# Optimization experiments

Measured on AMD Instinct MI355X. Metric: run time of the kernel, lower is better.

Reference implementation:

```python
import jax, jax.numpy as jnp
import numpy as np

DIM = 2048            # model dim
HID = 4096            # ssm inner dim (multiple_of*round(2/3*6144))
H = 64                # n_heads
P = HID // H          # head_dim = 64
N = 128               # state_dim
G = 1                 # n_groups
K = 4                 # conv_size
Q = 128               # chunk_size
CONV_DIM = HID + 2 * G * N       # 4352
D_IN = 2 * HID + 2 * G * N + H   # 8512
EPS = 1e-5


def _causal_conv_silu(xBC, w):
    # xBC: [B,L,C], w: [C,K]; depthwise causal conv1d fused with SiLU
    kern = w.T[:, None, :]  # [K,1,C]
    y = jax.lax.conv_general_dilated(
        xBC, kern, window_strides=(1,), padding=[(K - 1, 0)],
        dimension_numbers=('NHC', 'HIO', 'NHC'),
        feature_group_count=xBC.shape[-1])
    return y * jax.nn.sigmoid(y)


def _ssm(x, W_in, conv_w, dt_bias, A_log, D, norm_w, W_out):
    Bsz, L, _ = x.shape
    zxbcdt = x @ W_in.T                       # [B,L,D_IN]
    z = zxbcdt[..., :HID]                     # gate
    xBC = zxbcdt[..., HID:HID + CONV_DIM]
    dt_raw = zxbcdt[..., HID + CONV_DIM:]     # [B,L,H]

    xBC = _causal_conv_silu(xBC, conv_w)
    xs = xBC[..., :HID].reshape(Bsz, L, H, P)
    rep = H // G
    Bh = jnp.repeat(xBC[..., HID:HID + G * N].reshape(Bsz, L, G, N), rep, axis=2)  # [B,L,H,N]
    Ch = jnp.repeat(xBC[..., HID + G * N:].reshape(Bsz, L, G, N), rep, axis=2)

    dt = jax.nn.softplus(dt_raw + dt_bias)    # [B,L,H], dt_softplus=True
    A = -jnp.exp(A_log)                       # [H]

    # ---- chunked selective scan (Mamba2 SSD), chunk size Q ----
    nc = L // Q
    a = (dt * A).reshape(Bsz, nc, Q, H)
    cum = jnp.cumsum(a, axis=2)               # inclusive within-chunk cumsum, <= 0
    xs_c = xs.reshape(Bsz, nc, Q, H, P)
    dtc = dt.reshape(Bsz, nc, Q, H)
    Bc = Bh.reshape(Bsz, nc, Q, H, N)
    Cc = Ch.reshape(Bsz, nc, Q, H, N)

    # intra-chunk (diagonal) part: Y[i] += sum_{j<=i} exp(cum_i-cum_j) dt_j (C_i.B_j) x_j
    diff = cum[:, :, :, None, :] - cum[:, :, None, :, :]     # [b,c,i,j,h]
    tril = jnp.tril(jnp.ones((Q, Q), bool))[None, None, :, :, None]
    Lmat = jnp.exp(jnp.where(tril, diff, -jnp.inf))          # causal decay matrix
    CB = jnp.einsum('bcihn,bcjhn->bcijh', Cc, Bc)
    M = CB * Lmat * dtc[:, :, None, :, :]
    Yd = jnp.einsum('bcijh,bcjhp->bcihp', M, xs_c)

    # per-chunk end state: sum_j exp(cum_last-cum_j) dt_j x_j (x) B_j
    wdec = jnp.exp(cum[:, :, -1:, :] - cum) * dtc            # [b,c,q,h]
    states = jnp.einsum('bcqh,bcqhn,bcqhp->bchpn', wdec, Bc, xs_c)
    chunk_decay = jnp.exp(cum[:, :, -1, :])                  # [b,c,h]

    # inter-chunk recurrence over nc chunks
    def step(S, inp):
        dec, st = inp                                        # [b,h], [b,h,p,n]
        return S * dec[..., None, None] + st, S              # emit state entering chunk
    S0 = jnp.zeros((Bsz, H, P, N), x.dtype)
    _, Sprev = jax.lax.scan(step, S0,
                            (chunk_decay.transpose(1, 0, 2),
                             states.transpose(1, 0, 2, 3, 4)))
    Sprev = Sprev.transpose(1, 0, 2, 3, 4)                   # [b,c,h,p,n]

    # inter-chunk (off-diagonal) contribution
    Yoff = jnp.einsum('bcqh,bcqhn,bchpn->bcqhp', jnp.exp(cum), Cc, Sprev)

    y = (Yd + Yoff).reshape(Bsz, L, H, P) + D[None, None, :, None] * xs  # skip D
    y = y.reshape(Bsz, L, HID)

    yz = y * (z * jax.nn.sigmoid(z))                         # gated: y * silu(z)
    yn = yz * jax.lax.rsqrt(jnp.mean(yz * yz, axis=-1, keepdims=True) + EPS) * norm_w
    return yn @ W_out.T


def setup_inputs() -> dict:
    key = jax.random.key(0)
    k = jax.random.split(key, 6)
    return {
        'x': jax.random.normal(k[0], (2, 4096, DIM), jnp.float32),
        'W_in': jax.random.normal(k[1], (D_IN, DIM), jnp.float32) * DIM ** -0.5,
        'conv_w': jax.random.normal(k[2], (CONV_DIM, K), jnp.float32) * K ** -0.5,
        'dt_bias': jax.random.uniform(k[3], (H,), jnp.float32, minval=0.001, maxval=0.1),
        'A_log': jnp.log(jax.random.uniform(k[4], (H,), jnp.float32, minval=1.0, maxval=16.0)),
        'D': jnp.ones((H,), jnp.float32),
        'norm_w': jnp.ones((HID,), jnp.float32),
        'W_out': jax.random.normal(k[5], (DIM, HID), jnp.float32) * HID ** -0.5,
    }


def reference(x, W_in, conv_w, dt_bias, A_log, D, norm_w, W_out):
    return _ssm(x, W_in, conv_w, dt_bias, A_log, D, norm_w, W_out)
```

## Files before the change

kernel.cpp:

```cpp
#include <hip/hip_runtime.h>
#include <hip/hip_fp16.h>
#include <math.h>

#define ROWS   8192
#define DIMK   2048
#define HIDN   4096
#define QCH    128
#define NCHUNK 32

typedef __attribute__((ext_vector_type(8))) short short8;
typedef __attribute__((ext_vector_type(8))) _Float16 half8;
typedef __attribute__((ext_vector_type(4))) float floatx4;

static __device__ inline unsigned short f2h(float f){
  union { _Float16 h; unsigned short u; } v; v.h = (_Float16)f; return v.u;
}
static __device__ inline float h2f(unsigned short u){
  union { unsigned short u; _Float16 h; } v; v.u = u; return (float)v.h;
}
static __device__ inline void async_cp16(const void* g, void* l){
  __builtin_amdgcn_global_load_lds((const __attribute__((address_space(1))) void*)g,
                                   (__attribute__((address_space(3))) void*)l, 16, 0, 0);
}

__global__ void k_cast(const float* __restrict__ in, unsigned short* __restrict__ out, int n4){
  int i = blockIdx.x * 256 + threadIdx.x;
  if (i < n4){
    float4 v = ((const float4*)in)[i];
    unsigned long long p = (unsigned long long)f2h(v.x)
                         | ((unsigned long long)f2h(v.y) << 16)
                         | ((unsigned long long)f2h(v.z) << 32)
                         | ((unsigned long long)f2h(v.w) << 48);
    ((unsigned long long*)out)[i] = p;
  }
}

__global__ __launch_bounds__(256)
void k_dtraw(const float* __restrict__ x, const float* __restrict__ Win,
             float* __restrict__ dtraw){
  __shared__ float ws[64 * 132];
  const int t = threadIdx.x;
  const int lane = t & 63, w = t >> 6;
  const int r0 = blockIdx.x * 16;
  const int rw = __builtin_amdgcn_readfirstlane(r0 + w * 4);
  float a0 = 0.f, a1 = 0.f, a2 = 0.f, a3 = 0.f;
  for (int k0 = 0; k0 < DIMK; k0 += 128){
    __syncthreads();
#pragma unroll
    for (int l = 0; l < 8; l++){
      int fidx = (l * 256 + t) * 4;
      int row = fidx >> 7, col = fidx & 127;
      *(float4*)&ws[row * 132 + col] =
          *(const float4*)&Win[(size_t)(8448 + row) * DIMK + k0 + col];
    }
    __syncthreads();
    const float* xp = x + (size_t)rw * DIMK + k0;
#pragma unroll 8
    for (int kk = 0; kk < 128; kk += 4){
      float4 wv = *(const float4*)&ws[lane * 132 + kk];
      float4 v0 = *(const float4*)&xp[kk];
      float4 v1 = *(const float4*)&xp[DIMK + kk];
      float4 v2 = *(const float4*)&xp[2*DIMK + kk];
      float4 v3 = *(const float4*)&xp[3*DIMK + kk];
      a0 += wv.x*v0.x + wv.y*v0.y + wv.z*v0.z + wv.w*v0.w;
      a1 += wv.x*v1.x + wv.y*v1.y + wv.z*v1.z + wv.w*v1.w;
      a2 += wv.x*v2.x + wv.y*v2.y + wv.z*v2.z + wv.w*v2.w;
      a3 += wv.x*v3.x + wv.y*v3.y + wv.z*v3.z + wv.w*v3.w;
    }
  }
  dtraw[(size_t)rw * 64 + lane]       = a0;
  dtraw[((size_t)rw + 1) * 64 + lane] = a1;
  dtraw[((size_t)rw + 2) * 64 + lane] = a2;
  dtraw[((size_t)rw + 3) * 64 + lane] = a3;
}

static __device__ inline unsigned ldsaddr(const void* p){
  return (unsigned)(size_t)(const __attribute__((address_space(3))) void*)p;
}
static __device__ inline floatx4 dsr128(unsigned a){
  floatx4 d;
  asm volatile("ds_read_b128 %0, %1" : "=v"(d) : "v"(a));
  return d;
}
static __device__ inline half8 as_h8(floatx4 f){
  union { floatx4 f; half8 h; } u; u.f = f; return u.h;
}

template<int KD>
__device__ inline void gemm256_core(const unsigned short* __restrict__ A,
                                    const unsigned short* __restrict__ B,
                                    int row0, int col0,
                                    unsigned short* sA, unsigned short* sB,
                                    floatx4 (&acc)[8][4], int t){
  const int lane = t & 63, wid = t >> 6;
  const int wm = wid >> 2, wn = wid & 3;
  const int quad = lane >> 4, l16 = lane & 15;
  const int srow  = t >> 3;
  const int sslot = (t & 7) ^ (srow & 7);
  constexpr int NT = KD / 64;

  auto stageA = [&](int d, int half, int kt){
    unsigned short* dst = sA + d*256*64 + half*128*64;
    const unsigned short* src = A + (size_t)(row0 + half*128) * KD + kt*64;
#pragma unroll
    for (int i = 0; i < 2; i++)
      async_cp16(src + (size_t)(i*64 + srow) * KD + sslot*8,
                 dst + ((size_t)i*512 + t)*8);
  };
  auto stageB = [&](int d, int half, int kt){
    unsigned short* dst = sB + d*256*64 + half*128*64;
    const unsigned short* src = B + (size_t)(col0 + half*128) * KD + kt*64;
#pragma unroll
    for (int i = 0; i < 2; i++)
      async_cp16(src + (size_t)(i*64 + srow) * KD + sslot*8,
                 dst + ((size_t)i*512 + t)*8);
  };

  const unsigned sAbase = ldsaddr(sA), sBbase = ldsaddr(sB);
  floatx4 af[8][2], bf[4][2];
  auto rdA = [&](unsigned base, int fr, int ks) -> floatx4 {
    return dsr128(base + 2u*(unsigned)((fr*16 + l16)*64 + (((ks*4+quad)^(l16&7))*8)));
  };
  auto rdB = [&](unsigned base, int fc, int ks) -> floatx4 {
    return dsr128(base + 2u*(unsigned)((fc*16 + l16)*64 + (((ks*4+quad)^(l16&7))*8)));
  };
  auto mmac = [&](int mh, int nh){
    __builtin_amdgcn_s_setprio(1);
#pragma unroll
    for (int mm = 0; mm < 4; mm++)
#pragma unroll
      for (int nn = 0; nn < 2; nn++)
#pragma unroll
        for (int ks = 0; ks < 2; ks++)
          acc[mh*4+mm][nh*2+nn] = __builtin_amdgcn_mfma_f32_16x16x32_f16(
              as_h8(af[mh*4+mm][ks]), as_h8(bf[nh*2+nn][ks]), acc[mh*4+mm][nh*2+nn], 0, 0, 0);
    __builtin_amdgcn_s_setprio(0);
  };

  stageA(0,0,0); stageA(0,1,0); stageB(0,0,0); stageB(0,1,0);
  stageA(1,0,1); stageA(1,1,1);
  asm volatile("s_waitcnt vmcnt(4)" ::: "memory");
  __builtin_amdgcn_s_barrier();

  for (int T = 0; T < NT; T++){
    const int cur = T & 1;
    const unsigned aAd = sAbase + 2u*(unsigned)(cur*256*64 + wm*128*64);
    const unsigned bAd = sBbase + 2u*(unsigned)(cur*256*64 + wn*64*64);
#pragma unroll
    for (int fr = 0; fr < 4; fr++)
#pragma unroll
      for (int ks = 0; ks < 2; ks++)
        af[fr][ks] = rdA(aAd, fr, ks);
#pragma unroll
    for (int fc = 0; fc < 2; fc++)
#pragma unroll
      for (int ks = 0; ks < 2; ks++)
        bf[fc][ks] = rdB(bAd, fc, ks);
    if (T + 1 < NT) stageB(cur^1, 0, T+1);
    __builtin_amdgcn_s_barrier();
    asm volatile("s_waitcnt lgkmcnt(0)" ::: "memory");
    __builtin_amdgcn_sched_barrier(0);
    mmac(0, 0);
    __builtin_amdgcn_s_barrier();
#pragma unroll
    for (int fr = 4; fr < 8; fr++)
#pragma unroll
      for (int ks = 0; ks < 2; ks++)
        af[fr][ks] = rdA(aAd, fr, ks);
    if (T + 1 < NT) stageB(cur^1, 1, T+1);
    __builtin_amdgcn_s_barrier();
    asm volatile("s_waitcnt lgkmcnt(0)" ::: "memory");
    __builtin_amdgcn_sched_barrier(0);
    mmac(1, 0);
    __builtin_amdgcn_s_barrier();
#pragma unroll
    for (int fc = 2; fc < 4; fc++)
#pragma unroll
      for (int ks = 0; ks < 2; ks++)
        bf[fc][ks] = rdB(bAd, fc, ks);
    __builtin_amdgcn_s_barrier();
    asm volatile("s_waitcnt lgkmcnt(0)" ::: "memory");
    __builtin_amdgcn_sched_barrier(0);
    mmac(0, 1);
    __builtin_amdgcn_s_barrier();
    if (T + 2 < NT){
      stageA(cur, 0, T+2); stageA(cur, 1, T+2);
      asm volatile("s_waitcnt vmcnt(4)" ::: "memory");
    } else if (T + 1 < NT){
      asm volatile("s_waitcnt vmcnt(0)" ::: "memory");
    }
    __builtin_amdgcn_s_barrier();
    mmac(1, 1);
    __builtin_amdgcn_s_barrier();
  }
}

__global__ __launch_bounds__(512, 2)
void k_gemm1(const unsigned short* __restrict__ A, const unsigned short* __restrict__ B,
             unsigned short* __restrict__ zbuf, unsigned short* __restrict__ xsraw,
             unsigned short* __restrict__ bcraw){
  __shared__ __align__(16) unsigned short sA[2*256*64];
  __shared__ __align__(16) unsigned short sB[2*256*64];
  const int t = threadIdx.x;
  int swz = (blockIdx.x % 8) * 132 + blockIdx.x / 8;
  const int row0 = (swz & 31) * 256, col0 = (swz >> 5) * 256;
  floatx4 acc[8][4] = {};
  gemm256_core<DIMK>(A, B, row0, col0, sA, sB, acc, t);
  const int lane = t & 63, wid = t >> 6;
  const int wm = wid >> 2, wn = wid & 3;
  const int quad = lane >> 4, l16 = lane & 15;
  unsigned short* dst; int cbase, ldd;
  if (col0 < 4096){ dst = zbuf; cbase = 0; ldd = 4096; }
  else if (col0 < 8192){ dst = xsraw; cbase = 4096; ldd = 4096; }
  else { dst = bcraw; cbase = 8192; ldd = 256; }
#pragma unroll
  for (int m = 0; m < 8; m++)
#pragma unroll
    for (int n = 0; n < 4; n++){
      int rb = row0 + wm*128 + m*16 + quad*4;
      int cc = col0 + wn*64 + n*16 + l16 - cbase;
#pragma unroll
      for (int r = 0; r < 4; r++)
        dst[(size_t)(rb + r) * ldd + cc] = f2h(acc[m][n][r]);
    }
}

__global__ __launch_bounds__(512, 2)
void k_gemm2(const unsigned short* __restrict__ A, const unsigned short* __restrict__ B,
             float* __restrict__ C){
  __shared__ __align__(16) unsigned short sA[2*256*64];
  __shared__ __align__(16) unsigned short sB[2*256*64];
  const int t = threadIdx.x;
  int swz = (blockIdx.x % 8) * 32 + blockIdx.x / 8;
  const int row0 = (swz & 31) * 256, col0 = (swz >> 5) * 256;
  floatx4 acc[8][4] = {};
  gemm256_core<HIDN>(A, B, row0, col0, sA, sB, acc, t);
  const int lane = t & 63, wid = t >> 6;
  const int wm = wid >> 2, wn = wid & 3;
  const int quad = lane >> 4, l16 = lane & 15;
#pragma unroll
  for (int m = 0; m < 8; m++)
#pragma unroll
    for (int n = 0; n < 4; n++){
      int rb = row0 + wm*128 + m*16 + quad*4;
      int cc = col0 + wn*64 + n*16 + l16;
#pragma unroll
      for (int r = 0; r < 4; r++)
        C[(size_t)(rb + r) * DIMK + cc] = acc[m][n][r];
    }
}

__global__ void k_halo(const unsigned short* __restrict__ xsraw, unsigned short* __restrict__ halo){
  int col = blockIdx.x * 256 + threadIdx.x;
  int slot = blockIdx.y, bc = blockIdx.z;
  long r = (long)bc * QCH - 3 + slot;
  if (r >= 0)
    halo[((size_t)bc * 3 + slot) * 4096 + col] = xsraw[(size_t)r * 4096 + col];
}

__global__ void k_convbc(const unsigned short* __restrict__ bcraw, const float* __restrict__ cw,
                         unsigned short* __restrict__ bcc){
  int row = blockIdx.x, c = threadIdx.x;
  int tl = row & 4095;
  const float4 wv = *(const float4*)&cw[(size_t)(4096 + c) * 4];
  const unsigned short* col = bcraw + c;
  size_t rb = (size_t)row * 256;
  float a = h2f(col[rb]) * wv.w;
  if (tl >= 1) a += h2f(col[rb - 256]) * wv.z;
  if (tl >= 2) a += h2f(col[rb - 512]) * wv.y;
  if (tl >= 3) a += h2f(col[rb - 768]) * wv.x;
  bcc[rb + c] = f2h(a / (1.f + __expf(-a)));
}

__global__ void k_dtcum(const float* __restrict__ dtraw, const float* __restrict__ dtbias,
                        const float* __restrict__ Alog, float* __restrict__ dtb,
                        float* __restrict__ cumb){
  int bc = blockIdx.x;
  int h  = threadIdx.x;
  float bias = dtbias[h];
  float A = -__expf(Alog[h]);
  float run = 0.f;
  size_t rowb = (size_t)bc * QCH;
  for (int q = 0; q < QCH; q++){
    float dr = dtraw[(rowb + q) * 64 + h] + bias;
    float dt = dr > 20.f ? dr : log1pf(__expf(dr));
    dtb[(rowb + q) * 64 + h] = dt;
    run += dt * A;
    cumb[(rowb + q) * 64 + h] = run;
  }
}

__device__ inline void stage_xsT(const unsigned short* __restrict__ xsraw,
                                 const unsigned short* __restrict__ halo,
                                 const float* cws, unsigned short* xsT,
                                 int bc, int h, int t){
  const size_t rowb = (size_t)bc * QCH;
  const int tl0 = (bc & 31) * QCH;
#pragma unroll
  for (int it = 0; it < 2; it++){
    int idx = it * 256 + t;
    int q = idx & 127, p0 = (idx >> 7) * 16;
    int tl = tl0 + q;
    const unsigned short* cur = xsraw + (rowb + q) * 4096 + h * 64 + p0;
    const unsigned short* hb  = halo + ((size_t)bc * 3) * 4096 + h * 64 + p0;
    const unsigned short* r1 = (q >= 1) ? cur - 4096     : hb + 2 * 4096;
    const unsigned short* r2 = (q >= 2) ? cur - 2 * 4096 : hb + (size_t)(q + 1) * 4096;
    const unsigned short* r3 = (q >= 3) ? cur - 3 * 4096 : hb + (size_t)q * 4096;
    float f1 = (tl >= 1) ? 1.f : 0.f;
    float f2 = (tl >= 2) ? 1.f : 0.f;
    float f3 = (tl >= 3) ? 1.f : 0.f;
    short8 c0 = *(const short8*)cur, c1 = *(const short8*)(cur + 8);
    short8 a0 = *(const short8*)r1,  a1 = *(const short8*)(r1 + 8);
    short8 b0 = *(const short8*)r2,  b1 = *(const short8*)(r2 + 8);
    short8 d0 = *(const short8*)r3,  d1 = *(const short8*)(r3 + 8);
#pragma unroll
    for (int j = 0; j < 16; j++){
      int col = p0 + j;
      const float* wp = cws + col * 4;
      float vc = h2f((unsigned short)(j < 8 ? c0[j] : c1[j-8]));
      float v1 = h2f((unsigned short)(j < 8 ? a0[j] : a1[j-8]));
      float v2 = h2f((unsigned short)(j < 8 ? b0[j] : b1[j-8]));
      float v3 = h2f((unsigned short)(j < 8 ? d0[j] : d1[j-8]));
      float a = vc * wp[3] + f1 * v1 * wp[2] + f2 * v2 * wp[1] + f3 * v3 * wp[0];
      float s = a / (1.f + __expf(-a));
      xsT[col * 128 + q] = f2h(s);
    }
  }
}

__global__ __launch_bounds__(256, 2)
void k_chunk1(const unsigned short* __restrict__ xsc, const unsigned short* __restrict__ bcc,
              const float* __restrict__ dtb, const float* __restrict__ cumb,
              const float* __restrict__ Dp, const unsigned short* __restrict__ st,
              unsigned short* __restrict__ ybuf){
  __shared__ __align__(16) unsigned short Ml[128*128];
  __shared__ __align__(16) unsigned short xsT[64*128];
  __shared__ float cum_s[128], dt_s[128];
  const int blk = blockIdx.x, h = blk & 63, bc = blk >> 6;
  const size_t rowb = (size_t)bc * QCH;
  const int t = threadIdx.x, w = t >> 6, lane = t & 63, quad = lane >> 4, l16 = lane & 15;
  const int wrow = w * 32;
  if (t < 128){ cum_s[t] = cumb[(rowb + t)*64 + h]; dt_s[t] = dtb[(rowb + t)*64 + h]; }
  __syncthreads();
#pragma unroll
  for (int it = 0; it < 2; it++){
    int idx = it * 256 + t;
    int q = idx & 127, p0 = (idx >> 7) * 16;
    const unsigned short* cur = xsc + (rowb + q) * 4096 + h * 64 + p0;
    short8 c0 = *(const short8*)cur, c1 = *(const short8*)(cur + 8);
#pragma unroll
    for (int j = 0; j < 16; j++)
      xsT[(p0 + j) * 128 + q] = (unsigned short)(j < 8 ? c0[j] : c1[j-8]);
  }
  floatx4 acc[2][8] = {};
  const unsigned short* Cb = bcc + rowb * 256 + 128;
  const unsigned short* Bb = bcc + rowb * 256;
#pragma unroll
  for (int ks = 0; ks < 4; ks++){
    half8 af[2];
#pragma unroll
    for (int i = 0; i < 2; i++)
      af[i] = *(const half8*)(Cb + (size_t)(wrow + i*16 + l16) * 256 + ks*32 + quad*8);
#pragma unroll
    for (int j = 0; j < 8; j++){
      half8 bfr = *(const half8*)(Bb + (size_t)(j*16 + l16) * 256 + ks*32 + quad*8);
#pragma unroll
      for (int i = 0; i < 2; i++)
        acc[i][j] = __builtin_amdgcn_mfma_f32_16x16x32_f16(af[i], bfr, acc[i][j], 0, 0, 0);
    }
  }
#pragma unroll
  for (int i = 0; i < 2; i++)
#pragma unroll
    for (int j = 0; j < 8; j++){
      int jc = j*16 + l16;
      float dtj = dt_s[jc], cj = cum_s[jc];
#pragma unroll
      for (int r = 0; r < 4; r++){
        int ir = wrow + i*16 + quad*4 + r;
        float m = (ir >= jc) ? acc[i][j][r] * __expf(cum_s[ir] - cj) * dtj : 0.f;
        Ml[ir * 128 + jc] = f2h(m);
      }
    }
  __syncthreads();
  floatx4 accY[2][4] = {};
#pragma unroll
  for (int ks = 0; ks < 4; ks++){
    half8 af[2], bfr[4];
#pragma unroll
    for (int i = 0; i < 2; i++)
      af[i] = *(const half8*)&Ml[(wrow + i*16 + l16)*128 + ks*32 + quad*8];
#pragma unroll
    for (int p = 0; p < 4; p++)
      bfr[p] = *(const half8*)&xsT[(p*16 + l16)*128 + ks*32 + quad*8];
#pragma unroll
    for (int i = 0; i < 2; i++)
#pragma unroll
      for (int p = 0; p < 4; p++)
        accY[i][p] = __builtin_amdgcn_mfma_f32_16x16x32_f16(af[i], bfr[p], accY[i][p], 0, 0, 0);
  }
  __syncthreads();
  unsigned short* Sp = Ml;
  {
    size_t base = ((size_t)bc * 64 + h) * 8192;
#pragma unroll
    for (int it = 0; it < 4; it++){
      int idx = (it * 256 + t) * 8;
      *(short8*)&Sp[idx] = *(const short8*)&st[base + idx];
    }
  }
  __syncthreads();
  floatx4 accO[2][4] = {};
#pragma unroll
  for (int ks = 0; ks < 4; ks++){
    half8 af[2], bfr[4];
#pragma unroll
    for (int i = 0; i < 2; i++)
      af[i] = *(const half8*)(Cb + (size_t)(wrow + i*16 + l16) * 256 + ks*32 + quad*8);
#pragma unroll
    for (int p = 0; p < 4; p++)
      bfr[p] = *(const half8*)&Sp[(p*16 + l16)*128 + ks*32 + quad*8];
#pragma unroll
    for (int i = 0; i < 2; i++)
#pragma unroll
      for (int p = 0; p < 4; p++)
        accO[i][p] = __builtin_amdgcn_mfma_f32_16x16x32_f16(af[i], bfr[p], accO[i][p], 0, 0, 0);
  }
  float Dh = Dp[h];
#pragma unroll
  for (int i = 0; i < 2; i++)
#pragma unroll
    for (int p = 0; p < 4; p++){
      int pc = p*16 + l16;
#pragma unroll
      for (int r = 0; r < 4; r++){
        int ir = wrow + i*16 + quad*4 + r;
        float y = accY[i][p][r] + __expf(cum_s[ir]) * accO[i][p][r] + Dh * h2f(xsT[pc*128 + ir]);
        ybuf[(rowb + ir) * (size_t)HIDN + h*64 + pc] = f2h(y);
      }
    }
}

__global__ __launch_bounds__(256, 2)
void k_chunk2(unsigned short* __restrict__ xsraw, const unsigned short* __restrict__ bcc,
              const unsigned short* __restrict__ halo, const float* __restrict__ cw,
              const float* __restrict__ dtb, const float* __restrict__ cumb,
              unsigned short* __restrict__ st){
  __shared__ __align__(16) unsigned short wBT[128*128];
  __shared__ __align__(16) unsigned short xsT[64*128];
  __shared__ float cum_s[128], dt_s[128];
  __shared__ float cws[64*4];
  const int blk = blockIdx.x, h = blk & 63, bc = blk >> 6;
  const size_t rowb = (size_t)bc * QCH;
  const int t = threadIdx.x, w = t >> 6, lane = t & 63, quad = lane >> 4, l16 = lane & 15;
  if (t < 128){ cum_s[t] = cumb[(rowb + t)*64 + h]; dt_s[t] = dtb[(rowb + t)*64 + h]; }
  if (t < 64) *(float4*)&cws[t*4] = *(const float4*)&cw[((size_t)h*64 + t)*4];
  __syncthreads();
  stage_xsT(xsraw, halo, cws, xsT, bc, h, t);
  __syncthreads();
#pragma unroll
  for (int it = 0; it < 2; it++){
    int idx = it * 256 + t;
    int q = idx & 127, p0 = (idx >> 7) * 16;
    short8 w0, w1;
#pragma unroll
    for (int j = 0; j < 8; j++){
      w0[j] = (short)xsT[(p0 + j) * 128 + q];
      w1[j] = (short)xsT[(p0 + 8 + j) * 128 + q];
    }
    unsigned short* g = xsraw + (rowb + q) * 4096 + h * 64 + p0;
    *(short8*)g = w0;
    *(short8*)(g + 8) = w1;
  }
  float clast = cum_s[127];
#pragma unroll
  for (int it = 0; it < 2; it++){
    int idx = it * 256 + t;
    int q = idx & 127, n0 = (idx >> 7) * 32;
    float wd = __expf(clast - cum_s[q]) * dt_s[q];
    const unsigned short* gp = bcc + (rowb + q) * 256 + n0;
#pragma unroll
    for (int c4 = 0; c4 < 4; c4++){
      short8 v = *(const short8*)(gp + c4*8);
#pragma unroll
      for (int jj = 0; jj < 8; jj++)
        wBT[(n0 + c4*8 + jj)*128 + q] = f2h(h2f((unsigned short)v[jj]) * wd);
    }
  }
  __syncthreads();
  floatx4 acc[8] = {};
#pragma unroll
  for (int ks = 0; ks < 4; ks++){
    half8 af = *(const half8*)&xsT[(w*16 + l16)*128 + ks*32 + quad*8];
#pragma unroll
    for (int j = 0; j < 8; j++){
      half8 bfr = *(const half8*)&wBT[(j*16 + l16)*128 + ks*32 + quad*8];
      acc[j] = __builtin_amdgcn_mfma_f32_16x16x32_f16(af, bfr, acc[j], 0, 0, 0);
    }
  }
  size_t base = ((size_t)bc * 64 + h) * 8192;
#pragma unroll
  for (int j = 0; j < 8; j++){
    int n = j*16 + l16;
#pragma unroll
    for (int r = 0; r < 4; r++){
      int p = w*16 + quad*4 + r;
      st[base + p*128 + n] = f2h(acc[j][r]);
    }
  }
}

__global__ void k_scan(unsigned short* __restrict__ st, const float* __restrict__ cumb){
  int id = blockIdx.x * 256 + threadIdx.x;
  int n = id & 127, p = (id >> 7) & 63, h = (id >> 13) & 63, b = id >> 19;
  float S = 0.f;
  for (int c = 0; c < NCHUNK; c++){
    int bc = b * NCHUNK + c;
    size_t idx = ((size_t)bc * 64 + h) * 8192 + (size_t)p * 128 + n;
    float dec = __expf(cumb[((size_t)bc * QCH + 127) * 64 + h]);
    float v = h2f(st[idx]);
    st[idx] = f2h(S);
    S = S * dec + v;
  }
}

__global__ __launch_bounds__(256)
void k_gate(unsigned short* __restrict__ yb, const unsigned short* __restrict__ zb,
            const float* __restrict__ nw){
  __shared__ float red[4];
  int row = blockIdx.x, t = threadIdx.x;
  float vals[16], ss = 0.f;
#pragma unroll
  for (int it = 0; it < 16; it++){
    int c = it * 256 + t;
    float y = h2f(yb[(size_t)row * HIDN + c]);
    float z = h2f(zb[(size_t)row * HIDN + c]);
    float v = y * (z / (1.f + __expf(-z)));
    vals[it] = v; ss += v * v;
  }
  for (int o = 32; o > 0; o >>= 1) ss += __shfl_down(ss, o, 64);
  int w = t >> 6, lane = t & 63;
  if (lane == 0) red[w] = ss;
  __syncthreads();
  float scale = rsqrtf((red[0] + red[1] + red[2] + red[3]) / (float)HIDN + 1e-5f);
#pragma unroll
  for (int it = 0; it < 16; it++){
    int c = it * 256 + t;
    yb[(size_t)row * HIDN + c] = f2h(vals[it] * scale * nw[c]);
  }
}

extern "C" void kernel_launch(void* const* d_in, const int* in_sizes, int n_in,
                              void* d_out, int out_size, void* d_ws, size_t ws_size,
                              hipStream_t stream){
  const float* x      = (const float*)d_in[0];
  const float* Win    = (const float*)d_in[1];
  const float* convw  = (const float*)d_in[2];
  const float* dtbias = (const float*)d_in[3];
  const float* Alog   = (const float*)d_in[4];
  const float* Dp     = (const float*)d_in[5];
  const float* nw     = (const float*)d_in[6];
  const float* Wout   = (const float*)d_in[7];
  float* out = (float*)d_out;

  char* ws = (char*)d_ws;
  size_t off = 0;
  auto alloc = [&](size_t bytes)->void*{ void* p = ws + off; off += (bytes + 255) & ~(size_t)255; return p; };
  unsigned short* xw    = (unsigned short*)alloc((size_t)ROWS * DIMK * 2);
  unsigned short* winb  = (unsigned short*)alloc((size_t)8448 * DIMK * 2);
  float*          dtraw = (float*)alloc((size_t)ROWS * 64 * 4);
  unsigned short* woutb = (unsigned short*)alloc((size_t)DIMK * HIDN * 2);
  unsigned short* zbuf  = (unsigned short*)alloc((size_t)ROWS * HIDN * 2);
  unsigned short* xsraw = (unsigned short*)alloc((size_t)ROWS * HIDN * 2);
  unsigned short* bcraw = (unsigned short*)alloc((size_t)ROWS * 256 * 2);
  unsigned short* bcc   = (unsigned short*)alloc((size_t)ROWS * 256 * 2);
  unsigned short* halo  = (unsigned short*)alloc((size_t)64 * 3 * 4096 * 2);
  float*          dtb   = (float*)alloc((size_t)ROWS * 64 * 4);
  float*          cumb  = (float*)alloc((size_t)ROWS * 64 * 4);
  unsigned short* st    = xw;
  unsigned short* ybuf  = xsraw;

  k_cast<<<(ROWS*DIMK/4 + 255)/256, 256, 0, stream>>>(x, xw, ROWS*DIMK/4);
  k_cast<<<(8448*DIMK/4 + 255)/256, 256, 0, stream>>>(Win, winb, 8448*DIMK/4);
  k_cast<<<(DIMK*HIDN/4 + 255)/256, 256, 0, stream>>>(Wout, woutb, DIMK*HIDN/4);
  k_dtraw<<<ROWS/16, 256, 0, stream>>>(x, Win, dtraw);
  k_gemm1<<<dim3(33*32), 512, 0, stream>>>(xw, winb, zbuf, xsraw, bcraw);
  k_halo<<<dim3(16, 3, 64), 256, 0, stream>>>(xsraw, halo);
  k_convbc<<<ROWS, 256, 0, stream>>>(bcraw, convw, bcc);
  k_dtcum<<<64, 64, 0, stream>>>(dtraw, dtbias, Alog, dtb, cumb);
  k_chunk2<<<4096, 256, 0, stream>>>(xsraw, bcc, halo, convw, dtb, cumb, st);
  k_scan<<<4096, 256, 0, stream>>>(st, cumb);
  k_chunk1<<<4096, 256, 0, stream>>>(xsraw, bcc, dtb, cumb, Dp, st, ybuf);
  k_gate<<<ROWS, 256, 0, stream>>>(ybuf, zbuf, nw);
  k_gemm2<<<dim3(8*32), 512, 0, stream>>>(ybuf, woutb, out);
}
```

Before: 1.092 ms.

## Rework GEMM core to 256x128 tiles with K=32 triple-buffered staging

Replaces the 256x256-tile, K=64 double-buffered GEMM core with a 256x128 tile, K=32 step and a three-stage LDS ring buffer for both projection GEMMs. Each wave now holds 4x4 accumulators instead of 8x4, and launch bounds allow 4 blocks per CU, aiming to raise occupancy and overlap loads with MFMA. gemm2 in particular had only 256 blocks before and now gets 512, giving better CU fill. The cost is lower arithmetic intensity per tile, more barriers per unit of work, and a different swizzle mapping.

Result: slower. 1.238 ms (+13.4%).

```diff
diff --git a/kernel.cpp b/kernel.cpp
--- a/kernel.cpp
+++ b/kernel.cpp
@@ -87,137 +87,94 @@
 }
 
 template<int KD>
-__device__ inline void gemm256_core(const unsigned short* __restrict__ A,
-                                    const unsigned short* __restrict__ B,
-                                    int row0, int col0,
-                                    unsigned short* sA, unsigned short* sB,
-                                    floatx4 (&acc)[8][4], int t){
+__device__ inline void gemm_core32(const unsigned short* __restrict__ A,
+                                   const unsigned short* __restrict__ B,
+                                   int row0, int col0,
+                                   unsigned short* sA, unsigned short* sB,
+                                   floatx4 (&acc)[4][4], int t){
   const int lane = t & 63, wid = t >> 6;
-  const int wm = wid >> 2, wn = wid & 3;
+  const int wm = wid >> 1, wn = wid & 1;
   const int quad = lane >> 4, l16 = lane & 15;
-  const int srow  = t >> 3;
-  const int sslot = (t & 7) ^ (srow & 7);
-  constexpr int NT = KD / 64;
-
-  auto stageA = [&](int d, int half, int kt){
-    unsigned short* dst = sA + d*256*64 + half*128*64;
-    const unsigned short* src = A + (size_t)(row0 + half*128) * KD + kt*64;
+  constexpr int NT = KD / 32;
+  const int sr  = t >> 2;
+  const int ssl = (t & 3) ^ ((t >> 3) & 3);
+
+  auto stageA = [&](int b, int kt){
+    unsigned short* dst = sA + b*8192;
+    const unsigned short* src = A + (size_t)row0 * KD + kt*32 + ssl*8;
 #pragma unroll
     for (int i = 0; i < 2; i++)
-      async_cp16(src + (size_t)(i*64 + srow) * KD + sslot*8,
-                 dst + ((size_t)i*512 + t)*8);
+      async_cp16(src + (size_t)(i*128 + sr) * KD, dst + ((size_t)i*512 + t)*8);
   };
-  auto stageB = [&](int d, int half, int kt){
-    unsigned short* dst = sB + d*256*64 + half*128*64;
-    const unsigned short* src = B + (size_t)(col0 + half*128) * KD + kt*64;
-#pragma unroll
-    for (int i = 0; i < 2; i++)
-      async_cp16(src + (size_t)(i*64 + srow) * KD + sslot*8,
-                 dst + ((size_t)i*512 + t)*8);
+  auto stageB = [&](int b, int kt){
+    unsigned short* dst = sB + b*4096;
+    const unsigned short* src = B + (size_t)col0 * KD + kt*32 + ssl*8;
+    async_cp16(src + (size_t)sr * KD, dst + (size_t)t*8);
   };
 
-  const unsigned sAbase = ldsaddr(sA), sBbase = ldsaddr(sB);
-  floatx4 af[8][2], bf[4][2];
-  auto rdA = [&](unsigned base, int fr, int ks) -> floatx4 {
-    return dsr128(base + 2u*(unsigned)((fr*16 + l16)*64 + (((ks*4+quad)^(l16&7))*8)));
-  };
-  auto rdB = [&](unsigned base, int fc, int ks) -> floatx4 {
-    return dsr128(base + 2u*(unsigned)((fc*16 + l16)*64 + (((ks*4+quad)^(l16&7))*8)));
-  };
-  auto mmac = [&](int mh, int nh){
-    __builtin_amdgcn_s_setprio(1);
-#pragma unroll
-    for (int mm = 0; mm < 4; mm++)
-#pragma unroll
-      for (int nn = 0; nn < 2; nn++)
-#pragma unroll
-        for (int ks = 0; ks < 2; ks++)
-          acc[mh*4+mm][nh*2+nn] = __builtin_amdgcn_mfma_f32_16x16x32_f16(
-              as_h8(af[mh*4+mm][ks]), as_h8(bf[nh*2+nn][ks]), acc[mh*4+mm][nh*2+nn], 0, 0, 0);
-    __builtin_amdgcn_s_setprio(0);
-  };
-
-  stageA(0,0,0); stageA(0,1,0); stageB(0,0,0); stageB(0,1,0);
-  stageA(1,0,1); stageA(1,1,1);
-  asm volatile("s_waitcnt vmcnt(4)" ::: "memory");
+  const unsigned sAb = ldsaddr(sA), sBb = ldsaddr(sB);
+  const unsigned rsw = (unsigned)((quad ^ ((l16 >> 1) & 3)) * 8);
+  floatx4 af[4], bf[4];
+
+  stageA(0,0); stageB(0,0);
+  stageA(1,1); stageB(1,1);
+  asm volatile("s_waitcnt vmcnt(3)" ::: "memory");
   __builtin_amdgcn_s_barrier();
 
+  int b = 0;
   for (int T = 0; T < NT; T++){
-    const int cur = T & 1;
-    const unsigned aAd = sAbase + 2u*(unsigned)(cur*256*64 + wm*128*64);
-    const unsigned bAd = sBbase + 2u*(unsigned)(cur*256*64 + wn*64*64);
-#pragma unroll
-    for (int fr = 0; fr < 4; fr++)
-#pragma unroll
-      for (int ks = 0; ks < 2; ks++)
-        af[fr][ks] = rdA(aAd, fr, ks);
-#pragma unroll
-    for (int fc = 0; fc < 2; fc++)
-#pragma unroll
-      for (int ks = 0; ks < 2; ks++)
-        bf[fc][ks] = rdB(bAd, fc, ks);
-    if (T + 1 < NT) stageB(cur^1, 0, T+1);
+    const unsigned aBase = sAb + 2u*((unsigned)(b*8192 + (wm*64 + l16)*32) + rsw);
+    const unsigned bBase = sBb + 2u*((unsigned)(b*4096 + (wn*64 + l16)*32) + rsw);
+#pragma unroll
+    for (int m = 0; m < 4; m++) af[m] = dsr128(aBase + 2u*(unsigned)(m*16*32));
+#pragma unroll
+    for (int n = 0; n < 4; n++) bf[n] = dsr128(bBase + 2u*(unsigned)(n*16*32));
+    int b2 = b + 2; if (b2 >= 3) b2 -= 3;
+    if (T + 2 < NT){
+      stageA(b2, T+2); stageB(b2, T+2);
+      asm volatile("s_waitcnt vmcnt(3)" ::: "memory");
+    } else if (T + 1 < NT){
+      asm volatile("s_waitcnt vmcnt(0)" ::: "memory");
+    }
     __builtin_amdgcn_s_barrier();
     asm volatile("s_waitcnt lgkmcnt(0)" ::: "memory");
     __builtin_amdgcn_sched_barrier(0);
-    mmac(0, 0);
+    __builtin_amdgcn_s_setprio(1);
+#pragma unroll
+    for (int m = 0; m < 4; m++)
+#pragma unroll
+      for (int n = 0; n < 4; n++)
+        acc[m][n] = __builtin_amdgcn_mfma_f32_16x16x32_f16(
+            as_h8(af[m]), as_h8(bf[n]), acc[m][n], 0, 0, 0);
+    __builtin_amdgcn_s_setprio(0);
     __builtin_amdgcn_s_barrier();
-#pragma unroll
-    for (int fr = 4; fr < 8; fr++)
-#pragma unroll
-      for (int ks = 0; ks < 2; ks++)
-        af[fr][ks] = rdA(aAd, fr, ks);
-    if (T + 1 < NT) stageB(cur^1, 1, T+1);
-    __builtin_amdgcn_s_barrier();
-    asm volatile("s_waitcnt lgkmcnt(0)" ::: "memory");
-    __builtin_amdgcn_sched_barrier(0);
-    mmac(1, 0);
-    __builtin_amdgcn_s_barrier();
-#pragma unroll
-    for (int fc = 2; fc < 4; fc++)
-#pragma unroll
-      for (int ks = 0; ks < 2; ks++)
-        bf[fc][ks] = rdB(bAd, fc, ks);
-    __builtin_amdgcn_s_barrier();
-    asm volatile("s_waitcnt lgkmcnt(0)" ::: "memory");
-    __builtin_amdgcn_sched_barrier(0);
-    mmac(0, 1);
-    __builtin_amdgcn_s_barrier();
-    if (T + 2 < NT){
-      stageA(cur, 0, T+2); stageA(cur, 1, T+2);
-      asm volatile("s_waitcnt vmcnt(4)" ::: "memory");
-    } else if (T + 1 < NT){
-      asm volatile("s_waitcnt vmcnt(0)" ::: "memory");
-    }
-    __builtin_amdgcn_s_barrier();
-    mmac(1, 1);
-    __builtin_amdgcn_s_barrier();
-  }
-}
-
-__global__ __launch_bounds__(512, 2)
+    b = b + 1; if (b >= 3) b = 0;
+  }
+}
+
+__global__ __launch_bounds__(512, 4)
 void k_gemm1(const unsigned short* __restrict__ A, const unsigned short* __restrict__ B,
              unsigned short* __restrict__ zbuf, unsigned short* __restrict__ xsraw,
              unsigned short* __restrict__ bcraw){
-  __shared__ __align__(16) unsigned short sA[2*256*64];
-  __shared__ __align__(16) unsigned short sB[2*256*64];
+  __shared__ __align__(16) unsigned short sA[3*256*32];
+  __shared__ __align__(16) unsigned short sB[3*128*32];
   const int t = threadIdx.x;
-  int swz = (blockIdx.x % 8) * 132 + blockIdx.x / 8;
-  const int row0 = (swz & 31) * 256, col0 = (swz >> 5) * 256;
-  floatx4 acc[8][4] = {};
-  gemm256_core<DIMK>(A, B, row0, col0, sA, sB, acc, t);
+  int swz = (blockIdx.x % 8) * 264 + blockIdx.x / 8;
+  const int row0 = (swz & 31) * 256, col0 = (swz >> 5) * 128;
+  floatx4 acc[4][4] = {};
+  gemm_core32<DIMK>(A, B, row0, col0, sA, sB, acc, t);
   const int lane = t & 63, wid = t >> 6;
-  const int wm = wid >> 2, wn = wid & 3;
+  const int wm = wid >> 1, wn = wid & 1;
   const int quad = lane >> 4, l16 = lane & 15;
   unsigned short* dst; int cbase, ldd;
   if (col0 < 4096){ dst = zbuf; cbase = 0; ldd = 4096; }
   else if (col0 < 8192){ dst = xsraw; cbase = 4096; ldd = 4096; }
   else { dst = bcraw; cbase = 8192; ldd = 256; }
 #pragma unroll
-  for (int m = 0; m < 8; m++)
+  for (int m = 0; m < 4; m++)
 #pragma unroll
     for (int n = 0; n < 4; n++){
-      int rb = row0 + wm*128 + m*16 + quad*4;
+      int rb = row0 + wm*64 + m*16 + quad*4;
       int cc = col0 + wn*64 + n*16 + l16 - cbase;
 #pragma unroll
       for (int r = 0; r < 4; r++)
@@ -225,24 +182,24 @@
     }
 }
 
-__global__ __launch_bounds__(512, 2)
+__global__ __launch_bounds__(512, 4)
 void k_gemm2(const unsigned short* __restrict__ A, const unsigned short* __restrict__ B,
              float* __restrict__ C){
-  __shared__ __align__(16) unsigned short sA[2*256*64];
-  __shared__ __align__(16) unsigned short sB[2*256*64];
+  __shared__ __align__(16) unsigned short sA[3*256*32];
+  __shared__ __align__(16) unsigned short sB[3*128*32];
   const int t = threadIdx.x;
-  int swz = (blockIdx.x % 8) * 32 + blockIdx.x / 8;
-  const int row0 = (swz & 31) * 256, col0 = (swz >> 5) * 256;
-  floatx4 acc[8][4] = {};
-  gemm256_core<HIDN>(A, B, row0, col0, sA, sB, acc, t);
+  int swz = (blockIdx.x % 8) * 64 + blockIdx.x / 8;
+  const int row0 = (swz & 31) * 256, col0 = (swz >> 5) * 128;
+  floatx4 acc[4][4] = {};
+  gemm_core32<HIDN>(A, B, row0, col0, sA, sB, acc, t);
   const int lane = t & 63, wid = t >> 6;
-  const int wm = wid >> 2, wn = wid & 3;
+  const int wm = wid >> 1, wn = wid & 1;
   const int quad = lane >> 4, l16 = lane & 15;
 #pragma unroll
-  for (int m = 0; m < 8; m++)
+  for (int m = 0; m < 4; m++)
 #pragma unroll
     for (int n = 0; n < 4; n++){
-      int rb = row0 + wm*128 + m*16 + quad*4;
+      int rb = row0 + wm*64 + m*16 + quad*4;
       int cc = col0 + wn*64 + n*16 + l16;
 #pragma unroll
       for (int r = 0; r < 4; r++)
@@ -584,7 +541,7 @@
   k_cast<<<(8448*DIMK/4 + 255)/256, 256, 0, stream>>>(Win, winb, 8448*DIMK/4);
   k_cast<<<(DIMK*HIDN/4 + 255)/256, 256, 0, stream>>>(Wout, woutb, DIMK*HIDN/4);
   k_dtraw<<<ROWS/16, 256, 0, stream>>>(x, Win, dtraw);
-  k_gemm1<<<dim3(33*32), 512, 0, stream>>>(xw, winb, zbuf, xsraw, bcraw);
+  k_gemm1<<<dim3(32*66), 512, 0, stream>>>(xw, winb, zbuf, xsraw, bcraw);
   k_halo<<<dim3(16, 3, 64), 256, 0, stream>>>(xsraw, halo);
   k_convbc<<<ROWS, 256, 0, stream>>>(bcraw, convw, bcc);
   k_dtcum<<<64, 64, 0, stream>>>(dtraw, dtbias, Alog, dtb, cumb);
@@ -592,5 +549,5 @@
   k_scan<<<4096, 256, 0, stream>>>(st, cumb);
   k_chunk1<<<4096, 256, 0, stream>>>(xsraw, bcc, dtb, cumb, Dp, st, ybuf);
   k_gate<<<ROWS, 256, 0, stream>>>(ybuf, zbuf, nw);
-  k_gemm2<<<dim3(8*32), 512, 0, stream>>>(ybuf, woutb, out);
-}
+  k_gemm2<<<dim3(32*16), 512, 0, stream>>>(ybuf, woutb, out);
+}
```
